# Optimization experiments

Hardware: AMD Instinct MI355X
Metric: run time of the kernel (lower is better)

The kernel has to match this reference:

```python
import jax, jax.numpy as jnp
import numpy as np

N = 50000          # nodes
E = 800000         # edges (avg degree 16)
IN, HID, OUT = 128, 128, 64
LAMBDA_MAX = 2.0   # DGL default convention for scaled Laplacian (re_norm = 2/lambda_max = 1)


def setup_inputs() -> dict:
    key = jax.random.key(0)
    k1, k2, k3, k4, k5 = jax.random.split(key, 5)
    features = jax.random.normal(k1, (N, IN), dtype=jnp.float32)
    src = jax.random.randint(k2, (E,), 0, N)
    dst = jax.random.randint(k3, (E,), 0, N)
    # ChebConv(k=2) linear: Linear(2*in, out), torch default uniform init
    s1 = 1.0 / np.sqrt(2 * IN)
    W1 = jax.random.uniform(k4, (2 * IN, HID), jnp.float32, -s1, s1)
    b1 = jnp.zeros((HID,), jnp.float32)
    s2 = 1.0 / np.sqrt(2 * HID)
    W2 = jax.random.uniform(k5, (2 * HID, OUT), jnp.float32, -s2, s2)
    b2 = jnp.zeros((OUT,), jnp.float32)
    return {"features": features, "src": src, "dst": dst,
            "W1": W1, "b1": b1, "W2": W2, "b2": b2}


def _cheb_conv(x, src, dst, d_invsqrt, W, b, re_norm):
    msg = (x * d_invsqrt)[src]                                   # [E, d]
    h = jax.ops.segment_sum(msg, dst, num_segments=N) * d_invsqrt  # [N, d]
    # X_1 = L_tilde X_0 = -re_norm * A_hat X + (re_norm - 1) * X
    x1 = -re_norm * h + x * (re_norm - 1.0)
    xt = jnp.concatenate([x, x1], axis=1)                        # [N, 2d]
    return xt @ W + b


def reference(features, src, dst, W1, b1, W2, b2):
    deg = jax.ops.segment_sum(jnp.ones((E,), jnp.float32), dst, num_segments=N)
    d_invsqrt = jnp.power(jnp.clip(deg, 1.0, None), -0.5)[:, None]  # [N,1]
    re_norm = 2.0 / LAMBDA_MAX
    h = _cheb_conv(features, src, dst, d_invsqrt, W1, b1, re_norm)
    # dropout omitted (eval mode)
    h = _cheb_conv(h, src, dst, d_invsqrt, W2, b2, re_norm)
    return h
```

## Files before the change

kernel.cpp:

```cpp
#include <hip/hip_runtime.h>

#define IN_DIM  128

typedef __bf16 bf16x8 __attribute__((ext_vector_type(8)));
typedef float  f32x4  __attribute__((ext_vector_type(4)));

static inline size_t align256(size_t x) { return (x + 255) & ~size_t(255); }

__device__ __forceinline__ ushort f2b1(float f) {
    union { float f; uint u; } c; c.f = f;
    uint u = c.u;
    uint r = (u + 0x7FFFu + ((u >> 16) & 1u)) >> 16;
    return (ushort)r;
}
__device__ __forceinline__ float b2f(uint v16) {
    union { uint u; float f; } c; c.u = v16 << 16; return c.f;
}


__global__ void zero_kernel(int4* __restrict__ p, int n16) {
    int i = blockIdx.x * blockDim.x + threadIdx.x;
    if (i < n16) p[i] = make_int4(0, 0, 0, 0);
}

__global__ void hist_kernel(const int* __restrict__ dst, int* __restrict__ deg,
                            int* __restrict__ rank, int E) {
    int e = blockIdx.x * blockDim.x + threadIdx.x;
    if (e < E) rank[e] = atomicAdd(&deg[dst[e]], 1);
}

__global__ __launch_bounds__(256) void scan_blocks(const int* __restrict__ deg,
                                                   int* __restrict__ pre,
                                                   int* __restrict__ bsum, int n) {
    __shared__ int sh[256];
    int t = threadIdx.x;
    int base = blockIdx.x * 1024 + t * 4;
    int v0 = 0, v1 = 0, v2 = 0, v3 = 0;
    if (base + 3 < n) {
        int4 v = *reinterpret_cast<const int4*>(deg + base);
        v0 = v.x; v1 = v.y; v2 = v.z; v3 = v.w;
    } else {
        if (base     < n) v0 = deg[base];
        if (base + 1 < n) v1 = deg[base + 1];
        if (base + 2 < n) v2 = deg[base + 2];
        if (base + 3 < n) v3 = deg[base + 3];
    }
    int s = v0 + v1 + v2 + v3;
    sh[t] = s;
    __syncthreads();
    for (int off = 1; off < 256; off <<= 1) {
        int x = (t >= off) ? sh[t - off] : 0;
        __syncthreads();
        sh[t] += x;
        __syncthreads();
    }
    int excl = sh[t] - s;
    if (t == 255) bsum[blockIdx.x] = sh[255];
    if (base     < n) pre[base]     = excl;
    if (base + 1 < n) pre[base + 1] = excl + v0;
    if (base + 2 < n) pre[base + 2] = excl + v0 + v1;
    if (base + 3 < n) pre[base + 3] = excl + v0 + v1 + v2;
}

__global__ void scan_bsum(int* __restrict__ bsum, int nb) {
    int l = threadIdx.x;
    int orig = (l < nb) ? bsum[l] : 0;
    int v = orig;
    for (int off = 1; off < 64; off <<= 1) {
        int u = __shfl_up(v, off);
        if (l >= off) v += u;
    }
    if (l < nb) bsum[l] = v - orig;
}

__global__ void scan_add(const int* __restrict__ pre, const int* __restrict__ bsum,
                         const int* __restrict__ deg,
                         int* __restrict__ rowptr, float* __restrict__ dinv,
                         int n, int E) {
    int i = blockIdx.x * blockDim.x + threadIdx.x;
    if (i < n) {
        rowptr[i] = pre[i] + bsum[i >> 10];
        int d = deg[i]; if (d < 1) d = 1;
        dinv[i] = rsqrtf((float)d);
    }
    if (i == 0) rowptr[n] = E;
}

template <typename CT>
__global__ __launch_bounds__(256) void fill_kernel(
    const int* __restrict__ src, const int* __restrict__ dst,
    const int* __restrict__ rowptr, const int* __restrict__ rank,
    CT* __restrict__ col, int E)
{
    int e0 = (blockIdx.x * blockDim.x + threadIdx.x) * 4;
    if (e0 + 3 < E) {
        int4 d4 = *reinterpret_cast<const int4*>(dst + e0);
        int4 r4 = *reinterpret_cast<const int4*>(rank + e0);
        int4 s4 = *reinterpret_cast<const int4*>(src + e0);
        int p0 = rowptr[d4.x] + r4.x;
        int p1 = rowptr[d4.y] + r4.y;
        int p2 = rowptr[d4.z] + r4.z;
        int p3 = rowptr[d4.w] + r4.w;
        col[p0] = (CT)s4.x;
        col[p1] = (CT)s4.y;
        col[p2] = (CT)s4.z;
        col[p3] = (CT)s4.w;
    } else {
        for (int e = e0; e < E; ++e)
            col[rowptr[dst[e]] + rank[e]] = (CT)src[e];
    }
}


__global__ __launch_bounds__(256) void conv_fused(
    const float* __restrict__ feats, ushort* __restrict__ featb, int nbF,
    const float* __restrict__ W1, ushort* __restrict__ W1t,
    const float* __restrict__ W2, ushort* __restrict__ W2ct)
{
    int b = blockIdx.x, t = threadIdx.x;
    if (b < nbF) {
        size_t i = ((size_t)b * 256 + t) * 4;
        float4 v = *reinterpret_cast<const float4*>(feats + i);
        ushort4 o;
        o.x = f2b1(v.x); o.y = f2b1(v.y); o.z = f2b1(v.z); o.w = f2b1(v.w);
        *reinterpret_cast<ushort4*>(featb + i) = o;
    } else if (b < nbF + 128) {
        int i = (b - nbF) * 256 + t;
        int k = i >> 7, c = i & 127;
        W1t[(size_t)c * 256 + k] = f2b1(W1[i]);
    } else {
        int i = (b - nbF - 128) * 256 + t;
        int c = i >> 7, k = i & 127;
        float v = (c < 64) ? W2[(size_t)k * 64 + c]
                           : W2[(size_t)(128 + k) * 64 + (c - 64)];
        W2ct[(size_t)c * 128 + k] = f2b1(v);
    }
}


__device__ __forceinline__ void gather16(
    const uint* __restrict__ Xu, int lane, int slane, int wlane, int coff,
    float& a0, float& a1)
{
    uint v[16]; float w[16];
    #pragma unroll
    for (int j = 0; j < 16; ++j) {
        int s  = __builtin_amdgcn_readlane(slane, coff + j);
        int wb = __builtin_amdgcn_readlane(wlane, coff + j);
        w[j] = __int_as_float(wb);
        v[j] = Xu[(size_t)s * 64 + lane];
    }
    #pragma unroll
    for (int j = 0; j < 16; ++j) {
        a0 += b2f(v[j] & 0xffffu) * w[j];
        a1 += b2f(v[j] >> 16) * w[j];
    }
}

template <typename CT>
__global__ __launch_bounds__(256) void agg_bf16(
    const ushort* __restrict__ X, const int* __restrict__ rowptr,
    const CT* __restrict__ col, const float* __restrict__ dinv,
    ushort* __restrict__ X1, int nNodes)
{
    int wid  = (blockIdx.x * blockDim.x + threadIdx.x) >> 6;
    int lane = threadIdx.x & 63;
    if (wid >= nNodes) return;
    int e0 = rowptr[wid], e1 = rowptr[wid + 1];
    float sc = -dinv[wid];
    const uint* Xu = reinterpret_cast<const uint*>(X);

    float a0 = 0.f, a1 = 0.f;
    for (int base = e0; base < e1; base += 64) {
        int idx = base + lane;
        int cl = (idx < e1) ? idx : (e1 - 1);
        int s = (int)col[cl];
        float w = (idx < e1) ? dinv[s] : 0.f;
        int wlane = __float_as_int(w);
        int cnt = e1 - base; if (cnt > 64) cnt = 64;
        gather16(Xu, lane, s, wlane, 0, a0, a1);
        if (cnt > 16) gather16(Xu, lane, s, wlane, 16, a0, a1);
        if (cnt > 32) gather16(Xu, lane, s, wlane, 32, a0, a1);
        if (cnt > 48) gather16(Xu, lane, s, wlane, 48, a0, a1);
    }
    uint o = (uint)f2b1(a0 * sc) | ((uint)f2b1(a1 * sc) << 16);
    reinterpret_cast<uint*>(X1)[(size_t)wid * 64 + lane] = o;
}


__device__ __forceinline__ void gather16z(
    const ushort* __restrict__ Z, int lane, int slane, int wlane, int coff, float& a0)
{
    uint v[16]; float w[16];
    #pragma unroll
    for (int j = 0; j < 16; ++j) {
        int s  = __builtin_amdgcn_readlane(slane, coff + j);
        int wb = __builtin_amdgcn_readlane(wlane, coff + j);
        w[j] = __int_as_float(wb);
        v[j] = Z[(size_t)s * 64 + lane];
    }
    #pragma unroll
    for (int j = 0; j < 16; ++j)
        a0 += b2f(v[j]) * w[j];
}

template <typename CT>
__global__ __launch_bounds__(256) void agg_add64(
    const ushort* __restrict__ Z2, const int* __restrict__ rowptr,
    const CT* __restrict__ col, const float* __restrict__ dinv,
    float* __restrict__ Y, int nNodes)
{
    int wid  = (blockIdx.x * blockDim.x + threadIdx.x) >> 6;
    int lane = threadIdx.x & 63;
    if (wid >= nNodes) return;
    int e0 = rowptr[wid], e1 = rowptr[wid + 1];
    float sc = -dinv[wid];

    float a0 = 0.f;
    for (int base = e0; base < e1; base += 64) {
        int idx = base + lane;
        int cl = (idx < e1) ? idx : (e1 - 1);
        int s = (int)col[cl];
        float w = (idx < e1) ? dinv[s] : 0.f;
        int wlane = __float_as_int(w);
        int cnt = e1 - base; if (cnt > 64) cnt = 64;
        gather16z(Z2, lane, s, wlane, 0, a0);
        if (cnt > 16) gather16z(Z2, lane, s, wlane, 16, a0);
        if (cnt > 32) gather16z(Z2, lane, s, wlane, 32, a0);
        if (cnt > 48) gather16z(Z2, lane, s, wlane, 48, a0);
    }
    Y[(size_t)wid * 64 + lane] += a0 * sc;
}


__global__ __launch_bounds__(256) void gemm_mfma1(
    const ushort* __restrict__ XA, const ushort* __restrict__ XB,
    const ushort* __restrict__ Wt, const float* __restrict__ bias,
    ushort* __restrict__ Y, int nNodes)
{
    __shared__ ushort wlds[128 * 256];
    int t = threadIdx.x;

    #pragma unroll
    for (int it = 0; it < 16; ++it) {
        int i = it * 256 + t;
        int c = i >> 5;
        int o = (i & 31) << 4;
        bf16x8 v = *reinterpret_cast<const bf16x8*>(Wt + ((size_t)c << 8) + (o >> 1));
        *reinterpret_cast<bf16x8*>((char*)wlds + ((size_t)c << 9) + (o ^ ((c & 7) << 4))) = v;
    }
    __syncthreads();

    int wave = t >> 6, lane = t & 63;
    int r16 = lane & 15, g = lane >> 4;
    int nodeBase = blockIdx.x * 128 + wave * 32;

    int arow0 = nodeBase + r16;       if (arow0 > nNodes - 1) arow0 = nNodes - 1;
    int arow1 = nodeBase + 16 + r16;  if (arow1 > nNodes - 1) arow1 = nNodes - 1;
    const ushort* pA0 = XA + (size_t)arow0 * 128;
    const ushort* pA1 = XA + (size_t)arow1 * 128;
    const ushort* pB0 = XB + (size_t)arow0 * 128;
    const ushort* pB1 = XB + (size_t)arow1 * 128;

    f32x4 acc0[8], acc1[8];
    #pragma unroll
    for (int i = 0; i < 8; ++i) { acc0[i] = f32x4{0,0,0,0}; acc1[i] = f32x4{0,0,0,0}; }

    #pragma unroll
    for (int kb = 0; kb < 8; ++kb) {
        int kk = (kb & 3) * 32 + g * 8;
        bf16x8 a0 = *reinterpret_cast<const bf16x8*>(((kb < 4) ? pA0 : pB0) + kk);
        bf16x8 a1 = *reinterpret_cast<const bf16x8*>(((kb < 4) ? pA1 : pB1) + kk);
        int o = kb * 64 + g * 16;
        #pragma unroll
        for (int ct = 0; ct < 8; ++ct) {
            int c = ct * 16 + r16;
            bf16x8 b = *reinterpret_cast<const bf16x8*>(
                (const char*)wlds + ((size_t)c << 9) + (o ^ ((c & 7) << 4)));
            acc0[ct] = __builtin_amdgcn_mfma_f32_16x16x32_bf16(a0, b, acc0[ct], 0, 0, 0);
            acc1[ct] = __builtin_amdgcn_mfma_f32_16x16x32_bf16(a1, b, acc1[ct], 0, 0, 0);
        }
    }

    #pragma unroll
    for (int ct = 0; ct < 8; ++ct) {
        float bv = bias[ct * 16 + r16];
        #pragma unroll
        for (int r = 0; r < 4; ++r) {
            int orow0 = nodeBase + g * 4 + r;
            int orow1 = orow0 + 16;
            if (orow0 < nNodes) Y[(size_t)orow0 * 128 + ct * 16 + r16] = f2b1(acc0[ct][r] + bv);
            if (orow1 < nNodes) Y[(size_t)orow1 * 128 + ct * 16 + r16] = f2b1(acc1[ct][r] + bv);
        }
    }
}


__global__ __launch_bounds__(256) void gemm_mfma2(
    const ushort* __restrict__ H1, const ushort* __restrict__ W2ct,
    const float* __restrict__ bias, float* __restrict__ Yout,
    ushort* __restrict__ Z2, int nNodes)
{
    __shared__ ushort wlds[128 * 128];
    int t = threadIdx.x;

    #pragma unroll
    for (int it = 0; it < 8; ++it) {
        int i = it * 256 + t;
        int c = i >> 4;
        int o = (i & 15) << 4;
        bf16x8 v = *reinterpret_cast<const bf16x8*>(W2ct + ((size_t)c << 7) + (o >> 1));
        *reinterpret_cast<bf16x8*>((char*)wlds + ((size_t)c << 8) + (o ^ ((c & 7) << 4))) = v;
    }
    __syncthreads();

    int wave = t >> 6, lane = t & 63;
    int r16 = lane & 15, g = lane >> 4;
    int nodeBase = blockIdx.x * 128 + wave * 32;

    int arow0 = nodeBase + r16;       if (arow0 > nNodes - 1) arow0 = nNodes - 1;
    int arow1 = nodeBase + 16 + r16;  if (arow1 > nNodes - 1) arow1 = nNodes - 1;
    const ushort* p0 = H1 + (size_t)arow0 * 128;
    const ushort* p1 = H1 + (size_t)arow1 * 128;

    f32x4 acc0[8], acc1[8];
    #pragma unroll
    for (int i = 0; i < 8; ++i) { acc0[i] = f32x4{0,0,0,0}; acc1[i] = f32x4{0,0,0,0}; }

    #pragma unroll
    for (int kb = 0; kb < 4; ++kb) {
        int kk = kb * 32 + g * 8;
        bf16x8 a0 = *reinterpret_cast<const bf16x8*>(p0 + kk);
        bf16x8 a1 = *reinterpret_cast<const bf16x8*>(p1 + kk);
        int o = kb * 64 + g * 16;
        #pragma unroll
        for (int ct = 0; ct < 8; ++ct) {
            int c = ct * 16 + r16;
            bf16x8 b = *reinterpret_cast<const bf16x8*>(
                (const char*)wlds + ((size_t)c << 8) + (o ^ ((c & 7) << 4)));
            acc0[ct] = __builtin_amdgcn_mfma_f32_16x16x32_bf16(a0, b, acc0[ct], 0, 0, 0);
            acc1[ct] = __builtin_amdgcn_mfma_f32_16x16x32_bf16(a1, b, acc1[ct], 0, 0, 0);
        }
    }

    #pragma unroll
    for (int ct = 0; ct < 8; ++ct) {
        float bv = (ct < 4) ? bias[ct * 16 + r16] : 0.f;
        #pragma unroll
        for (int r = 0; r < 4; ++r) {
            int orow0 = nodeBase + g * 4 + r;
            int orow1 = orow0 + 16;
            if (ct < 4) {
                if (orow0 < nNodes) Yout[(size_t)orow0 * 64 + ct * 16 + r16] = acc0[ct][r] + bv;
                if (orow1 < nNodes) Yout[(size_t)orow1 * 64 + ct * 16 + r16] = acc1[ct][r] + bv;
            } else {
                if (orow0 < nNodes) Z2[(size_t)orow0 * 64 + (ct - 4) * 16 + r16] = f2b1(acc0[ct][r]);
                if (orow1 < nNodes) Z2[(size_t)orow1 * 64 + (ct - 4) * 16 + r16] = f2b1(acc1[ct][r]);
            }
        }
    }
}


extern "C" void kernel_launch(void* const* d_in, const int* in_sizes, int n_in,
                              void* d_out, int out_size, void* d_ws, size_t ws_size,
                              hipStream_t stream)
{
    const float* feats = (const float*)d_in[0];
    const int*   src   = (const int*)d_in[1];
    const int*   dst   = (const int*)d_in[2];
    const float* W1    = (const float*)d_in[3];
    const float* b1    = (const float*)d_in[4];
    const float* W2    = (const float*)d_in[5];
    const float* b2    = (const float*)d_in[6];
    float* out = (float*)d_out;

    const int N = in_sizes[0] / IN_DIM;
    const int E = in_sizes[1];
    const int NB = (N + 1023) / 1024;

    char* ws = (char*)d_ws;
    size_t off = 0;
    int*    deg    = (int*)(ws + off);    off = align256(off + (size_t)N * 4);
    int*    rowptr = (int*)(ws + off);    off = align256(off + (size_t)(N + 1) * 4);
    int*    pre    = (int*)(ws + off);    off = align256(off + (size_t)N * 4);
    int*    bsum   = (int*)(ws + off);    off = align256(off + (size_t)64 * 4);
    int*    rank   = (int*)(ws + off);    off = align256(off + (size_t)E * 4);
    void*   colv   = (void*)(ws + off);   off = align256(off + (size_t)E * 4);
    float*  dinv   = (float*)(ws + off);  off = align256(off + (size_t)N * 4);
    ushort* featb  = (ushort*)(ws + off); off = align256(off + (size_t)N * 128 * 2);
    ushort* x1b    = (ushort*)(ws + off); off = align256(off + (size_t)N * 128 * 2);
    ushort* h1b    = (ushort*)(ws + off); off = align256(off + (size_t)N * 128 * 2);
    ushort* z2b    = (ushort*)(ws + off); off = align256(off + (size_t)N * 64 * 2);
    ushort* W1t    = (ushort*)(ws + off); off = align256(off + (size_t)256 * 128 * 2);
    ushort* W2ct   = (ushort*)(ws + off); off = align256(off + (size_t)128 * 128 * 2);

    const int n16 = (N * 4 + 15) / 16;
    zero_kernel<<<(n16 + 255) / 256, 256, 0, stream>>>((int4*)deg, n16);
    hist_kernel<<<(E + 255) / 256, 256, 0, stream>>>(dst, deg, rank, E);
    scan_blocks<<<NB, 256, 0, stream>>>(deg, pre, bsum, N);
    scan_bsum<<<1, 64, 0, stream>>>(bsum, NB);
    scan_add<<<(N + 255) / 256, 256, 0, stream>>>(pre, bsum, deg, rowptr, dinv, N, E);

    const bool small = (N <= 65535);
    const int fillBlocks = ((E + 3) / 4 + 255) / 256;
    if (small)
        fill_kernel<ushort><<<fillBlocks, 256, 0, stream>>>(src, dst, rowptr, rank, (ushort*)colv, E);
    else
        fill_kernel<uint><<<fillBlocks, 256, 0, stream>>>(src, dst, rowptr, rank, (uint*)colv, E);

    const int nbF = (N * 128) / 1024;
    conv_fused<<<nbF + 128 + 64, 256, 0, stream>>>(feats, featb, nbF, W1, W1t, W2, W2ct);

    const int aggBlocks = (N * 64 + 255) / 256;
    const int gemmBlocks = (N + 127) / 128;

    if (small)
        agg_bf16<ushort><<<aggBlocks, 256, 0, stream>>>(featb, rowptr, (const ushort*)colv, dinv, x1b, N);
    else
        agg_bf16<uint><<<aggBlocks, 256, 0, stream>>>(featb, rowptr, (const uint*)colv, dinv, x1b, N);
    gemm_mfma1<<<gemmBlocks, 256, 0, stream>>>(featb, x1b, W1t, b1, h1b, N);

    gemm_mfma2<<<gemmBlocks, 256, 0, stream>>>(h1b, W2ct, b2, out, z2b, N);
    if (small)
        agg_add64<ushort><<<aggBlocks, 256, 0, stream>>>(z2b, rowptr, (const ushort*)colv, dinv, out, N);
    else
        agg_add64<uint><<<aggBlocks, 256, 0, stream>>>(z2b, rowptr, (const uint*)colv, dinv, out, N);
}
```

Measured before the change: 151.3 us.

## Prescale sources by D^-1/2 and fuse scan/fill/convert launches

Source rows are pre-multiplied by dinv: during feature conversion for layer 1, and in the GEMM2 epilogue for layer 2. The aggregation kernels therefore become plain sums, with no per-edge dinv gather or multiply. Padded lanes point at a zeroed sentinel row instead of using a weight of zero. The bsum scan is folded into scan_add, the CSR fill is merged with the conversion kernel to cut launches, and 32-bit indexing plus readfirstlane trim address arithmetic. The cost is an extra scaled bf16 copy of the features, which adds write traffic and a second rounding step.

```diff
diff --git a/kernel.cpp b/kernel.cpp
--- a/kernel.cpp
+++ b/kernel.cpp
@@ -13,8 +13,11 @@
     uint r = (u + 0x7FFFu + ((u >> 16) & 1u)) >> 16;
     return (ushort)r;
 }
-__device__ __forceinline__ float b2f(uint v16) {
-    union { uint u; float f; } c; c.u = v16 << 16; return c.f;
+__device__ __forceinline__ float lo_bf(uint v) {
+    union { uint u; float f; } c; c.u = v << 16; return c.f;
+}
+__device__ __forceinline__ float hi_bf(uint v) {
+    union { uint u; float f; } c; c.u = v & 0xffff0000u; return c.f;
 }
 
 
@@ -62,74 +65,85 @@
     if (base + 3 < n) pre[base + 3] = excl + v0 + v1 + v2;
 }
 
-__global__ void scan_bsum(int* __restrict__ bsum, int nb) {
-    int l = threadIdx.x;
-    int orig = (l < nb) ? bsum[l] : 0;
-    int v = orig;
-    for (int off = 1; off < 64; off <<= 1) {
-        int u = __shfl_up(v, off);
-        if (l >= off) v += u;
-    }
-    if (l < nb) bsum[l] = v - orig;
-}
-
-__global__ void scan_add(const int* __restrict__ pre, const int* __restrict__ bsum,
-                         const int* __restrict__ deg,
-                         int* __restrict__ rowptr, float* __restrict__ dinv,
-                         int n, int E) {
-    int i = blockIdx.x * blockDim.x + threadIdx.x;
+__global__ __launch_bounds__(256) void scan_add(
+    const int* __restrict__ pre, const int* __restrict__ bsum,
+    const int* __restrict__ deg,
+    int* __restrict__ rowptr, float* __restrict__ dinv,
+    int n, int E, int nb)
+{
+    __shared__ int sb[64];
+    int t = threadIdx.x;
+    if (t < 64) {
+        int orig = (t < nb) ? bsum[t] : 0;
+        int v = orig;
+        for (int off = 1; off < 64; off <<= 1) {
+            int u = __shfl_up(v, off);
+            if (t >= off) v += u;
+        }
+        sb[t] = v - orig;
+    }
+    __syncthreads();
+    int i = blockIdx.x * blockDim.x + t;
     if (i < n) {
-        rowptr[i] = pre[i] + bsum[i >> 10];
+        rowptr[i] = pre[i] + sb[i >> 10];
         int d = deg[i]; if (d < 1) d = 1;
         dinv[i] = rsqrtf((float)d);
     }
     if (i == 0) rowptr[n] = E;
 }
 
+
 template <typename CT>
-__global__ __launch_bounds__(256) void fill_kernel(
+__global__ __launch_bounds__(256) void phase2_kernel(
     const int* __restrict__ src, const int* __restrict__ dst,
     const int* __restrict__ rowptr, const int* __restrict__ rank,
-    CT* __restrict__ col, int E)
-{
-    int e0 = (blockIdx.x * blockDim.x + threadIdx.x) * 4;
-    if (e0 + 3 < E) {
-        int4 d4 = *reinterpret_cast<const int4*>(dst + e0);
-        int4 r4 = *reinterpret_cast<const int4*>(rank + e0);
-        int4 s4 = *reinterpret_cast<const int4*>(src + e0);
-        int p0 = rowptr[d4.x] + r4.x;
-        int p1 = rowptr[d4.y] + r4.y;
-        int p2 = rowptr[d4.z] + r4.z;
-        int p3 = rowptr[d4.w] + r4.w;
-        col[p0] = (CT)s4.x;
-        col[p1] = (CT)s4.y;
-        col[p2] = (CT)s4.z;
-        col[p3] = (CT)s4.w;
-    } else {
-        for (int e = e0; e < E; ++e)
-            col[rowptr[dst[e]] + rank[e]] = (CT)src[e];
-    }
-}
-
-
-__global__ __launch_bounds__(256) void conv_fused(
-    const float* __restrict__ feats, ushort* __restrict__ featb, int nbF,
+    CT* __restrict__ col, int E, int fillBlocks,
+    const float* __restrict__ feats, const float* __restrict__ dinv,
+    ushort* __restrict__ featb, ushort* __restrict__ featbs,
+    ushort* __restrict__ z2s, int N, int nbF,
     const float* __restrict__ W1, ushort* __restrict__ W1t,
     const float* __restrict__ W2, ushort* __restrict__ W2ct)
 {
     int b = blockIdx.x, t = threadIdx.x;
-    if (b < nbF) {
-        size_t i = ((size_t)b * 256 + t) * 4;
-        float4 v = *reinterpret_cast<const float4*>(feats + i);
-        ushort4 o;
-        o.x = f2b1(v.x); o.y = f2b1(v.y); o.z = f2b1(v.z); o.w = f2b1(v.w);
-        *reinterpret_cast<ushort4*>(featb + i) = o;
-    } else if (b < nbF + 128) {
-        int i = (b - nbF) * 256 + t;
+    if (b < fillBlocks) {
+        int e0 = (b * 256 + t) * 4;
+        if (e0 + 3 < E) {
+            int4 d4 = *reinterpret_cast<const int4*>(dst + e0);
+            int4 r4 = *reinterpret_cast<const int4*>(rank + e0);
+            int4 s4 = *reinterpret_cast<const int4*>(src + e0);
+            col[rowptr[d4.x] + r4.x] = (CT)s4.x;
+            col[rowptr[d4.y] + r4.y] = (CT)s4.y;
+            col[rowptr[d4.z] + r4.z] = (CT)s4.z;
+            col[rowptr[d4.w] + r4.w] = (CT)s4.w;
+        } else {
+            for (int e = e0; e < E; ++e)
+                col[rowptr[dst[e]] + rank[e]] = (CT)src[e];
+        }
+        return;
+    }
+    int b2 = b - fillBlocks;
+    if (b2 < nbF) {
+        size_t i4 = (size_t)b2 * 256 + t;
+        if (i4 < (size_t)N * 32) {
+            size_t i = i4 * 4;
+            float4 v = *reinterpret_cast<const float4*>(feats + i);
+            float dv = dinv[i >> 7];
+            ushort4 o, os;
+            o.x  = f2b1(v.x);      o.y  = f2b1(v.y);      o.z  = f2b1(v.z);      o.w  = f2b1(v.w);
+            os.x = f2b1(v.x * dv); os.y = f2b1(v.y * dv); os.z = f2b1(v.z * dv); os.w = f2b1(v.w * dv);
+            *reinterpret_cast<ushort4*>(featb  + i) = o;
+            *reinterpret_cast<ushort4*>(featbs + i) = os;
+        }
+    } else if (b2 < nbF + 128) {
+        if (b2 == nbF) {
+            if (t < 32) *reinterpret_cast<uint2*>(featbs + (size_t)N * 128 + t * 4) = make_uint2(0, 0);
+            else if (t < 48) *reinterpret_cast<uint2*>(z2s + (size_t)N * 64 + (t - 32) * 4) = make_uint2(0, 0);
+        }
+        int i = (b2 - nbF) * 256 + t;
         int k = i >> 7, c = i & 127;
         W1t[(size_t)c * 256 + k] = f2b1(W1[i]);
     } else {
-        int i = (b - nbF - 128) * 256 + t;
+        int i = (b2 - nbF - 128) * 256 + t;
         int c = i >> 7, k = i & 127;
         float v = (c < 64) ? W2[(size_t)k * 64 + c]
                            : W2[(size_t)(128 + k) * 64 + (c - 64)];
@@ -138,74 +152,68 @@
 }
 
 
-__device__ __forceinline__ void gather16(
-    const uint* __restrict__ Xu, int lane, int slane, int wlane, int coff,
+__device__ __forceinline__ void sum16(
+    const uint* __restrict__ Xu, int lane, int slane, int coff,
     float& a0, float& a1)
 {
-    uint v[16]; float w[16];
+    uint v[16];
     #pragma unroll
     for (int j = 0; j < 16; ++j) {
-        int s  = __builtin_amdgcn_readlane(slane, coff + j);
-        int wb = __builtin_amdgcn_readlane(wlane, coff + j);
-        w[j] = __int_as_float(wb);
-        v[j] = Xu[(size_t)s * 64 + lane];
+        int s = __builtin_amdgcn_readlane(slane, coff + j);
+        v[j] = Xu[(uint)(s * 64 + lane)];
     }
     #pragma unroll
     for (int j = 0; j < 16; ++j) {
-        a0 += b2f(v[j] & 0xffffu) * w[j];
-        a1 += b2f(v[j] >> 16) * w[j];
+        a0 += lo_bf(v[j]);
+        a1 += hi_bf(v[j]);
     }
 }
 
 template <typename CT>
-__global__ __launch_bounds__(256) void agg_bf16(
-    const ushort* __restrict__ X, const int* __restrict__ rowptr,
+__global__ __launch_bounds__(256) void agg_sum128(
+    const ushort* __restrict__ Xs, const int* __restrict__ rowptr,
     const CT* __restrict__ col, const float* __restrict__ dinv,
     ushort* __restrict__ X1, int nNodes)
 {
     int wid  = (blockIdx.x * blockDim.x + threadIdx.x) >> 6;
     int lane = threadIdx.x & 63;
     if (wid >= nNodes) return;
+    wid = __builtin_amdgcn_readfirstlane(wid);
     int e0 = rowptr[wid], e1 = rowptr[wid + 1];
     float sc = -dinv[wid];
-    const uint* Xu = reinterpret_cast<const uint*>(X);
+    const uint* Xu = reinterpret_cast<const uint*>(Xs);
 
     float a0 = 0.f, a1 = 0.f;
     for (int base = e0; base < e1; base += 64) {
         int idx = base + lane;
-        int cl = (idx < e1) ? idx : (e1 - 1);
-        int s = (int)col[cl];
-        float w = (idx < e1) ? dinv[s] : 0.f;
-        int wlane = __float_as_int(w);
+        int s = (idx < e1) ? (int)col[(idx < e1) ? idx : e0] : nNodes;
         int cnt = e1 - base; if (cnt > 64) cnt = 64;
-        gather16(Xu, lane, s, wlane, 0, a0, a1);
-        if (cnt > 16) gather16(Xu, lane, s, wlane, 16, a0, a1);
-        if (cnt > 32) gather16(Xu, lane, s, wlane, 32, a0, a1);
-        if (cnt > 48) gather16(Xu, lane, s, wlane, 48, a0, a1);
+        sum16(Xu, lane, s, 0, a0, a1);
+        if (cnt > 16) sum16(Xu, lane, s, 16, a0, a1);
+        if (cnt > 32) sum16(Xu, lane, s, 32, a0, a1);
+        if (cnt > 48) sum16(Xu, lane, s, 48, a0, a1);
     }
     uint o = (uint)f2b1(a0 * sc) | ((uint)f2b1(a1 * sc) << 16);
-    reinterpret_cast<uint*>(X1)[(size_t)wid * 64 + lane] = o;
-}
-
-
-__device__ __forceinline__ void gather16z(
-    const ushort* __restrict__ Z, int lane, int slane, int wlane, int coff, float& a0)
-{
-    uint v[16]; float w[16];
+    reinterpret_cast<uint*>(X1)[(uint)(wid * 64 + lane)] = o;
+}
+
+
+__device__ __forceinline__ void sum16z(
+    const ushort* __restrict__ Z, int lane, int slane, int coff, float& a0)
+{
+    ushort v[16];
     #pragma unroll
     for (int j = 0; j < 16; ++j) {
-        int s  = __builtin_amdgcn_readlane(slane, coff + j);
-        int wb = __builtin_amdgcn_readlane(wlane, coff + j);
-        w[j] = __int_as_float(wb);
-        v[j] = Z[(size_t)s * 64 + lane];
+        int s = __builtin_amdgcn_readlane(slane, coff + j);
+        v[j] = Z[(uint)(s * 64 + lane)];
     }
     #pragma unroll
     for (int j = 0; j < 16; ++j)
-        a0 += b2f(v[j]) * w[j];
+        a0 += lo_bf((uint)v[j]);
 }
 
 template <typename CT>
-__global__ __launch_bounds__(256) void agg_add64(
+__global__ __launch_bounds__(256) void agg_sum64(
     const ushort* __restrict__ Z2, const int* __restrict__ rowptr,
     const CT* __restrict__ col, const float* __restrict__ dinv,
     float* __restrict__ Y, int nNodes)
@@ -213,23 +221,21 @@
     int wid  = (blockIdx.x * blockDim.x + threadIdx.x) >> 6;
     int lane = threadIdx.x & 63;
     if (wid >= nNodes) return;
+    wid = __builtin_amdgcn_readfirstlane(wid);
     int e0 = rowptr[wid], e1 = rowptr[wid + 1];
     float sc = -dinv[wid];
 
     float a0 = 0.f;
     for (int base = e0; base < e1; base += 64) {
         int idx = base + lane;
-        int cl = (idx < e1) ? idx : (e1 - 1);
-        int s = (int)col[cl];
-        float w = (idx < e1) ? dinv[s] : 0.f;
-        int wlane = __float_as_int(w);
+        int s = (idx < e1) ? (int)col[(idx < e1) ? idx : e0] : nNodes;
         int cnt = e1 - base; if (cnt > 64) cnt = 64;
-        gather16z(Z2, lane, s, wlane, 0, a0);
-        if (cnt > 16) gather16z(Z2, lane, s, wlane, 16, a0);
-        if (cnt > 32) gather16z(Z2, lane, s, wlane, 32, a0);
-        if (cnt > 48) gather16z(Z2, lane, s, wlane, 48, a0);
-    }
-    Y[(size_t)wid * 64 + lane] += a0 * sc;
+        sum16z(Z2, lane, s, 0, a0);
+        if (cnt > 16) sum16z(Z2, lane, s, 16, a0);
+        if (cnt > 32) sum16z(Z2, lane, s, 32, a0);
+        if (cnt > 48) sum16z(Z2, lane, s, 48, a0);
+    }
+    Y[(uint)(wid * 64 + lane)] += a0 * sc;
 }
 
 
@@ -298,8 +304,8 @@
 
 __global__ __launch_bounds__(256) void gemm_mfma2(
     const ushort* __restrict__ H1, const ushort* __restrict__ W2ct,
-    const float* __restrict__ bias, float* __restrict__ Yout,
-    ushort* __restrict__ Z2, int nNodes)
+    const float* __restrict__ bias, const float* __restrict__ dinv,
+    float* __restrict__ Yout, ushort* __restrict__ Z2, int nNodes)
 {
     __shared__ ushort wlds[128 * 128];
     int t = threadIdx.x;
@@ -343,6 +349,14 @@
         }
     }
 
+    float dv0[4], dv1[4];
+    #pragma unroll
+    for (int r = 0; r < 4; ++r) {
+        int o0 = nodeBase + g * 4 + r;      if (o0 > nNodes - 1) o0 = nNodes - 1;
+        int o1 = nodeBase + 16 + g * 4 + r; if (o1 > nNodes - 1) o1 = nNodes - 1;
+        dv0[r] = dinv[o0]; dv1[r] = dinv[o1];
+    }
+
     #pragma unroll
     for (int ct = 0; ct < 8; ++ct) {
         float bv = (ct < 4) ? bias[ct * 16 + r16] : 0.f;
@@ -354,8 +368,8 @@
                 if (orow0 < nNodes) Yout[(size_t)orow0 * 64 + ct * 16 + r16] = acc0[ct][r] + bv;
                 if (orow1 < nNodes) Yout[(size_t)orow1 * 64 + ct * 16 + r16] = acc1[ct][r] + bv;
             } else {
-                if (orow0 < nNodes) Z2[(size_t)orow0 * 64 + (ct - 4) * 16 + r16] = f2b1(acc0[ct][r]);
-                if (orow1 < nNodes) Z2[(size_t)orow1 * 64 + (ct - 4) * 16 + r16] = f2b1(acc1[ct][r]);
+                if (orow0 < nNodes) Z2[(size_t)orow0 * 64 + (ct - 4) * 16 + r16] = f2b1(acc0[ct][r] * dv0[r]);
+                if (orow1 < nNodes) Z2[(size_t)orow1 * 64 + (ct - 4) * 16 + r16] = f2b1(acc1[ct][r] * dv1[r]);
             }
         }
     }
@@ -389,41 +403,44 @@
     void*   colv   = (void*)(ws + off);   off = align256(off + (size_t)E * 4);
     float*  dinv   = (float*)(ws + off);  off = align256(off + (size_t)N * 4);
     ushort* featb  = (ushort*)(ws + off); off = align256(off + (size_t)N * 128 * 2);
+    ushort* featbs = (ushort*)(ws + off); off = align256(off + (size_t)(N + 1) * 128 * 2);
     ushort* x1b    = (ushort*)(ws + off); off = align256(off + (size_t)N * 128 * 2);
     ushort* h1b    = (ushort*)(ws + off); off = align256(off + (size_t)N * 128 * 2);
-    ushort* z2b    = (ushort*)(ws + off); off = align256(off + (size_t)N * 64 * 2);
+    ushort* z2s    = (ushort*)(ws + off); off = align256(off + (size_t)(N + 1) * 64 * 2);
     ushort* W1t    = (ushort*)(ws + off); off = align256(off + (size_t)256 * 128 * 2);
     ushort* W2ct   = (ushort*)(ws + off); off = align256(off + (size_t)128 * 128 * 2);
 
-    const int n16 = (N * 4 + 15) / 16;
+    const int n16 = (N + 3) / 4;
     zero_kernel<<<(n16 + 255) / 256, 256, 0, stream>>>((int4*)deg, n16);
     hist_kernel<<<(E + 255) / 256, 256, 0, stream>>>(dst, deg, rank, E);
     scan_blocks<<<NB, 256, 0, stream>>>(deg, pre, bsum, N);
-    scan_bsum<<<1, 64, 0, stream>>>(bsum, NB);
-    scan_add<<<(N + 255) / 256, 256, 0, stream>>>(pre, bsum, deg, rowptr, dinv, N, E);
+    scan_add<<<(N + 255) / 256, 256, 0, stream>>>(pre, bsum, deg, rowptr, dinv, N, E, NB);
 
     const bool small = (N <= 65535);
     const int fillBlocks = ((E + 3) / 4 + 255) / 256;
+    const int nbF = (N * 32 + 255) / 256;
+    const int p2Blocks = fillBlocks + nbF + 128 + 64;
     if (small)
-        fill_kernel<ushort><<<fillBlocks, 256, 0, stream>>>(src, dst, rowptr, rank, (ushort*)colv, E);
+        phase2_kernel<ushort><<<p2Blocks, 256, 0, stream>>>(
+            src, dst, rowptr, rank, (ushort*)colv, E, fillBlocks,
+            feats, dinv, featb, featbs, z2s, N, nbF, W1, W1t, W2, W2ct);
     else
-        fill_kernel<uint><<<fillBlocks, 256, 0, stream>>>(src, dst, rowptr, rank, (uint*)colv, E);
-
-    const int nbF = (N * 128) / 1024;
-    conv_fused<<<nbF + 128 + 64, 256, 0, stream>>>(feats, featb, nbF, W1, W1t, W2, W2ct);
+        phase2_kernel<uint><<<p2Blocks, 256, 0, stream>>>(
+            src, dst, rowptr, rank, (uint*)colv, E, fillBlocks,
+            feats, dinv, featb, featbs, z2s, N, nbF, W1, W1t, W2, W2ct);
 
     const int aggBlocks = (N * 64 + 255) / 256;
     const int gemmBlocks = (N + 127) / 128;
 
     if (small)
-        agg_bf16<ushort><<<aggBlocks, 256, 0, stream>>>(featb, rowptr, (const ushort*)colv, dinv, x1b, N);
+        agg_sum128<ushort><<<aggBlocks, 256, 0, stream>>>(featbs, rowptr, (const ushort*)colv, dinv, x1b, N);
     else
-        agg_bf16<uint><<<aggBlocks, 256, 0, stream>>>(featb, rowptr, (const uint*)colv, dinv, x1b, N);
+        agg_sum128<uint><<<aggBlocks, 256, 0, stream>>>(featbs, rowptr, (const uint*)colv, dinv, x1b, N);
     gemm_mfma1<<<gemmBlocks, 256, 0, stream>>>(featb, x1b, W1t, b1, h1b, N);
 
-    gemm_mfma2<<<gemmBlocks, 256, 0, stream>>>(h1b, W2ct, b2, out, z2b, N);
+    gemm_mfma2<<<gemmBlocks, 256, 0, stream>>>(h1b, W2ct, b2, dinv, out, z2s, N);
     if (small)
-        agg_add64<ushort><<<aggBlocks, 256, 0, stream>>>(z2b, rowptr, (const ushort*)colv, dinv, out, N);
+        agg_sum64<ushort><<<aggBlocks, 256, 0, stream>>>(z2s, rowptr, (const ushort*)colv, dinv, out, N);
     else
-        agg_add64<uint><<<aggBlocks, 256, 0, stream>>>(z2b, rowptr, (const uint*)colv, dinv, out, N);
-}
+        agg_sum64<uint><<<aggBlocks, 256, 0, stream>>>(z2s, rowptr, (const uint*)colv, dinv, out, N);
+}
```

Result: faster. 145.9 us (-3.6%).
